# Kernel tuning notes

Hardware: AMD Instinct MI355X
Metric: run time of the kernel (lower is better)

Reference implementation:

```python
import jax, jax.numpy as jnp
import numpy as np

H, D, KV, S, PAST, BS, NB = 32, 128, 8, 128, 8064, 128, 128
T = PAST + S          # total context = 8192
NBLK = T // BS        # logical blocks used = 64
NEG = jnp.float32(-1e30)


def setup_inputs() -> dict:
    key = jax.random.key(0)
    ks = jax.random.split(key, 6)
    q = jax.random.normal(ks[0], (1, H, S, D), jnp.float32)
    k = jax.random.normal(ks[1], (1, KV, S, D), jnp.float32)
    v = jax.random.normal(ks[2], (1, KV, S, D), jnp.float32)
    pk = jax.random.normal(ks[3], (NB, KV, BS, D), jnp.float32)
    pv = jax.random.normal(ks[4], (NB, KV, BS, D), jnp.float32)
    # block table: 64 logical blocks mapped to distinct physical blocks (paged indirection)
    bt = jax.random.permutation(ks[5], NB)[:NBLK].astype(jnp.int32)
    return dict(
        query_state=q, key_state=k, value_state=v,
        attn_mask=jnp.ones((1,), jnp.float32),  # unused: causal prefill path (use_attention_mask=False)
        past_key_state=pk, past_value_state=pv,
        seq_position=PAST,
        scale=jnp.float32(1.0 / np.sqrt(D)),
        block_tables=bt, block_size=BS,
    )


def reference(query_state, key_state, value_state, attn_mask,
              past_key_state, past_value_state, seq_position, scale,
              block_tables, block_size):
    # phase == 'prefill', use_attention_mask=False -> paged_causal_attn_prefill
    kvh = past_key_state.shape[1]
    s_new = query_state.shape[2]
    total = seq_position + s_new  # static python int

    # --- append new K/V into the paged cache at positions [seq_position, total) ---
    pos_new = seq_position + jnp.arange(s_new)
    blk = block_tables[pos_new // block_size]
    off = pos_new % block_size
    k_new = jnp.transpose(key_state[0], (1, 0, 2))    # [S, KV, D]
    v_new = jnp.transpose(value_state[0], (1, 0, 2))
    kc = past_key_state.at[blk, :, off, :].set(k_new)
    vc = past_value_state.at[blk, :, off, :].set(v_new)

    # --- gather the full context [0, total) through the block table ---
    pos = jnp.arange(total)
    blk_a = block_tables[pos // block_size]
    off_a = pos % block_size
    K = kc[blk_a, :, off_a, :]   # [T, KV, D]
    V = vc[blk_a, :, off_a, :]

    # --- grouped-query causal attention ---
    g = query_state.shape[1] // kvh
    q = query_state.reshape(kvh, g, s_new, -1)                 # [KV, G, S, D]
    scores = jnp.einsum('kgsd,tkd->kgst', q, K) * scale        # [KV, G, S, T]
    causal = pos[None, :] <= (seq_position + jnp.arange(s_new))[:, None]  # [S, T]
    scores = jnp.where(causal[None, None], scores, NEG)
    probs = jax.nn.softmax(scores, axis=-1)
    out = jnp.einsum('kgst,tkd->kgsd', probs, V)               # [KV, G, S, D]

    h = kvh * g
    out = out.reshape(1, h, s_new, -1)                         # [1, H, S, D]
    out = jnp.transpose(out, (0, 2, 1, 3)).reshape(1, s_new, h * out.shape[-1])
    return out
```

## Files before the change

kernel.cpp:

```cpp
#include <hip/hip_runtime.h>
#include <hip/hip_bf16.h>


typedef unsigned short u16;
typedef unsigned int u32;
typedef __bf16 bf16x8 __attribute__((ext_vector_type(8)));
typedef float f32x16 __attribute__((ext_vector_type(16)));
typedef float f32x4 __attribute__((ext_vector_type(4)));
typedef u32 u32x4 __attribute__((ext_vector_type(4)));
typedef u32 u32x2 __attribute__((ext_vector_type(2)));
typedef int i32x2 __attribute__((ext_vector_type(2)));

#define NHEAD 32
#define DH 128
#define NKV 8
#define SQ 128
#define PAST_T 8064
#define TOTAL_T 8192
#define BK 64
#define KSTR 136
#define VT_SZ 8192
#define WSPP (16384 + 256)
#define MSUB 17.3123405f

__device__ __forceinline__ u32 pk2f(float lo, float hi) {
  union {
    __hip_bfloat162 b;
    u32 u;
  } cv;
  cv.b = __float22bfloat162_rn(make_float2(lo, hi));
  return cv.u;
}

template <int NPART>
__global__ __launch_bounds__(512, 1) void flash_part(
    const float* __restrict__ q, const float* __restrict__ knew,
    const float* __restrict__ vnew, const float* __restrict__ pk,
    const float* __restrict__ pv, const int* __restrict__ btab,
    const float* __restrict__ scp, float* __restrict__ ws) {
  constexpr int CHUNK = TOTAL_T / NPART;
  constexpr int NITER = CHUNK / BK;
  __shared__ __attribute__((aligned(16))) u16 k_s[2 * BK * KSTR];
  __shared__ __attribute__((aligned(16))) u16 vt_s[2 * VT_SZ];
  __shared__ int bt_s[64];

  const int bid = blockIdx.x;
  const int kv = bid & 7;
  const int t = bid >> 3;
  const int p = t % NPART;
  const int gp = t / NPART;

  const int tid = threadIdx.x;
  const int wid = tid >> 6;
  const int lane = tid & 63;
  const int g2 = wid & 1;
  const int w = wid >> 1;
  const int h = kv * 4 + gp * 2 + g2;
  const int l31 = lane & 31, grp = lane >> 5;
  const int pstart = p * CHUNK;

  if (tid < 64) bt_s[tid] = btab[tid];
  const float qs = scp[0] * 1.44269504f;

  u32x4 qf[8];
  {
    const float* qp = q + ((size_t)(h * SQ + w * 32 + l31)) * DH;
#pragma unroll
    for (int st = 0; st < 8; ++st) {
      const f32x4 a = *(const f32x4*)(qp + st * 16 + grp * 8);
      const f32x4 b = *(const f32x4*)(qp + st * 16 + grp * 8 + 4);
      u32x4 f;
      f[0] = pk2f(a[0] * qs, a[1] * qs);
      f[1] = pk2f(a[2] * qs, a[3] * qs);
      f[2] = pk2f(b[0] * qs, b[1] * qs);
      f[3] = pk2f(b[2] * qs, b[3] * qs);
      qf[st] = f;
    }
  }

  f32x16 oacc[4];
#pragma unroll
  for (int i = 0; i < 4; ++i)
#pragma unroll
    for (int rr = 0; rr < 16; ++rr) oacc[i][rr] = 0.0f;
  float l_acc = 0.0f;

  __syncthreads();

  f32x4 kr0, kr1, kr2, kr3;
  float va[8], vb[8];
  const int kc4 = (tid & 31) * 4;
  const int ktrow = tid >> 5;
  const int vd = tid & 127;
  const int tb8a = tid >> 7;
  const int vofA =
      ((((vd >> 5) * 4 + (tb8a >> 1)) * 2 + (tb8a & 1)) * 32 + (vd & 31)) * 8;
  const int vofB =
      ((((vd >> 5) * 4 + ((tb8a + 4) >> 1)) * 2 + ((tb8a + 4) & 1)) * 32 +
       (vd & 31)) * 8;

  auto load_tile = [&](int it) {
    const int t0 = pstart + it * BK;
    const float *sk, *sv;
    if (t0 < PAST_T) {
      const size_t boff =
          (((size_t)bt_s[t0 >> 7] * NKV + kv) * 128 + (t0 & 127)) * (size_t)DH;
      sk = pk + boff;
      sv = pv + boff;
    } else {
      const size_t noff = ((size_t)kv * SQ + (t0 - PAST_T)) * (size_t)DH;
      sk = knew + noff;
      sv = vnew + noff;
    }
    kr0 = *(const f32x4*)(sk + (size_t)(ktrow + 0) * DH + kc4);
    kr1 = *(const f32x4*)(sk + (size_t)(ktrow + 16) * DH + kc4);
    kr2 = *(const f32x4*)(sk + (size_t)(ktrow + 32) * DH + kc4);
    kr3 = *(const f32x4*)(sk + (size_t)(ktrow + 48) * DH + kc4);
#pragma unroll
    for (int j = 0; j < 8; ++j)
      va[j] = sv[(size_t)(tb8a * 8 + j) * DH + vd];
#pragma unroll
    for (int j = 0; j < 8; ++j)
      vb[j] = sv[(size_t)((tb8a + 4) * 8 + j) * DH + vd];
  };
  auto store_tile = [&](int buf) {
    u16* ks = k_s + buf * (BK * KSTR);
    u16* vs = vt_s + buf * VT_SZ;
    {
      u32x2 pw;
      pw[0] = pk2f(kr0[0], kr0[1]);
      pw[1] = pk2f(kr0[2], kr0[3]);
      *(u32x2*)&ks[(ktrow + 0) * KSTR + kc4] = pw;
    }
    {
      u32x2 pw;
      pw[0] = pk2f(kr1[0], kr1[1]);
      pw[1] = pk2f(kr1[2], kr1[3]);
      *(u32x2*)&ks[(ktrow + 16) * KSTR + kc4] = pw;
    }
    {
      u32x2 pw;
      pw[0] = pk2f(kr2[0], kr2[1]);
      pw[1] = pk2f(kr2[2], kr2[3]);
      *(u32x2*)&ks[(ktrow + 32) * KSTR + kc4] = pw;
    }
    {
      u32x2 pw;
      pw[0] = pk2f(kr3[0], kr3[1]);
      pw[1] = pk2f(kr3[2], kr3[3]);
      *(u32x2*)&ks[(ktrow + 48) * KSTR + kc4] = pw;
    }
    {
      u32x4 wa;
#pragma unroll
      for (int jj = 0; jj < 4; ++jj) wa[jj] = pk2f(va[2 * jj], va[2 * jj + 1]);
      *(u32x4*)&vs[vofA] = wa;
    }
    {
      u32x4 wb;
#pragma unroll
      for (int jj = 0; jj < 4; ++jj) wb[jj] = pk2f(vb[2 * jj], vb[2 * jj + 1]);
      *(u32x4*)&vs[vofB] = wb;
    }
  };

  load_tile(0);
  store_tile(0);
  __syncthreads();

  for (int it = 0; it < NITER; ++it) {
    const int buf = it & 1;
    if (it + 1 < NITER) load_tile(it + 1);

    const u16* ks = k_s + buf * (BK * KSTR);
    const u16* vs = vt_s + buf * VT_SZ;
    const int t0 = pstart + it * BK;
    const int qcol = w * 32 + l31;

    f32x16 sacc0, sacc1;
#pragma unroll
    for (int rr = 0; rr < 16; ++rr) sacc0[rr] = 0.0f;
#pragma unroll
    for (int rr = 0; rr < 16; ++rr) sacc1[rr] = 0.0f;
    __builtin_amdgcn_s_setprio(1);
#pragma unroll
    for (int st = 0; st < 8; ++st) {
      const u32x4 kf0 = *(const u32x4*)&ks[l31 * KSTR + st * 16 + grp * 8];
      sacc0 = __builtin_amdgcn_mfma_f32_32x32x16_bf16(
          __builtin_bit_cast(bf16x8, kf0), __builtin_bit_cast(bf16x8, qf[st]),
          sacc0, 0, 0, 0);
      const u32x4 kf1 =
          *(const u32x4*)&ks[(l31 + 32) * KSTR + st * 16 + grp * 8];
      sacc1 = __builtin_amdgcn_mfma_f32_32x32x16_bf16(
          __builtin_bit_cast(bf16x8, kf1), __builtin_bit_cast(bf16x8, qf[st]),
          sacc1, 0, 0, 0);
    }
    __builtin_amdgcn_s_setprio(0);

#pragma unroll
    for (int ts = 0; ts < 2; ++ts) {
      const f32x16& sacc = ts ? sacc1 : sacc0;
      const int tb = t0 + ts * 32;

      float pr[16];
      if (tb > PAST_T - 32) {
#pragma unroll
        for (int rr = 0; rr < 16; ++rr) {
          const int trow = (rr & 3) + 8 * (rr >> 2) + 4 * grp;
          const float e = __builtin_amdgcn_exp2f(sacc[rr] - MSUB);
          pr[rr] = ((tb + trow - PAST_T) > qcol) ? 0.0f : e;
        }
      } else {
#pragma unroll
        for (int rr = 0; rr < 16; ++rr)
          pr[rr] = __builtin_amdgcn_exp2f(sacc[rr] - MSUB);
      }
      float rs = 0.0f;
#pragma unroll
      for (int rr = 0; rr < 16; ++rr) rs += pr[rr];
      l_acc += rs;

      u32 pkk[8];
#pragma unroll
      for (int j = 0; j < 8; ++j) pkk[j] = pk2f(pr[2 * j], pr[2 * j + 1]);

      u32x4 pf1, pf2;
#if __has_builtin(__builtin_amdgcn_permlane32_swap)
      {
        const i32x2 s02 = __builtin_amdgcn_permlane32_swap(
            (int)pkk[0], (int)pkk[2], false, false);
        const i32x2 s13 = __builtin_amdgcn_permlane32_swap(
            (int)pkk[1], (int)pkk[3], false, false);
        const i32x2 s46 = __builtin_amdgcn_permlane32_swap(
            (int)pkk[4], (int)pkk[6], false, false);
        const i32x2 s57 = __builtin_amdgcn_permlane32_swap(
            (int)pkk[5], (int)pkk[7], false, false);
        pf1[0] = (u32)s02[0];
        pf1[1] = (u32)s13[0];
        pf1[2] = (u32)s02[1];
        pf1[3] = (u32)s13[1];
        pf2[0] = (u32)s46[0];
        pf2[1] = (u32)s57[0];
        pf2[2] = (u32)s46[1];
        pf2[3] = (u32)s57[1];
      }
#else
      {
        u32 xch[8];
#pragma unroll
        for (int j = 0; j < 8; ++j)
          xch[j] = (u32)__shfl_xor((int)pkk[j], 32, 64);
        pf1[0] = grp ? xch[2] : pkk[0];
        pf1[1] = grp ? xch[3] : pkk[1];
        pf1[2] = grp ? pkk[2] : xch[0];
        pf1[3] = grp ? pkk[3] : xch[1];
        pf2[0] = grp ? xch[6] : pkk[4];
        pf2[1] = grp ? xch[7] : pkk[5];
        pf2[2] = grp ? pkk[6] : xch[4];
        pf2[3] = grp ? pkk[7] : xch[5];
      }
#endif

      __builtin_amdgcn_s_setprio(1);
#pragma unroll
      for (int dt = 0; dt < 4; ++dt) {
        const u32x4 av =
            *(const u32x4*)&vs[((((dt * 4 + ts * 2) * 2 + grp) * 32 + l31)) * 8];
        oacc[dt] = __builtin_amdgcn_mfma_f32_32x32x16_bf16(
            __builtin_bit_cast(bf16x8, av), __builtin_bit_cast(bf16x8, pf1),
            oacc[dt], 0, 0, 0);
        const u32x4 bv =
            *(const u32x4*)&vs[((((dt * 4 + ts * 2 + 1) * 2 + grp) * 32 + l31)) *
                               8];
        oacc[dt] = __builtin_amdgcn_mfma_f32_32x32x16_bf16(
            __builtin_bit_cast(bf16x8, bv), __builtin_bit_cast(bf16x8, pf2),
            oacc[dt], 0, 0, 0);
      }
      __builtin_amdgcn_s_setprio(0);

      if (ts == 0 && it + 1 < NITER) store_tile(buf ^ 1);
    }

    __syncthreads();
  }

  float* wsp = ws + (size_t)(h * NPART + p) * WSPP;
#pragma unroll
  for (int dt = 0; dt < 4; ++dt)
#pragma unroll
    for (int rr = 0; rr < 16; ++rr) {
      const int dd = dt * 32 + (rr & 3) + 8 * (rr >> 2) + 4 * grp;
      wsp[dd * 128 + w * 32 + l31] = oacc[dt][rr];
    }
  const float l_tot = l_acc + __shfl_xor(l_acc, 32, 64);
  if (grp == 0) wsp[16384 + w * 32 + l31] = l_tot;
}

template <int NPART>
__global__ __launch_bounds__(256, 2) void combine_out(
    const float* __restrict__ ws, float* __restrict__ out) {
  __shared__ float rden_s[128];

  const int dblk = blockIdx.x;
  const int h = blockIdx.y;
  const int tid = threadIdx.x;
  const float* base = ws + (size_t)h * NPART * WSPP;

  if (tid < 128) {
    float denom = 0.0f;
#pragma unroll
    for (int pp = 0; pp < NPART; ++pp)
      denom += base[(size_t)pp * WSPP + 16384 + tid];
    rden_s[tid] = 1.0f / denom;
  }
  __syncthreads();

  const int qq = tid & 127;
  const int dp = tid >> 7;
  const int d0 = dblk * 4 + dp * 2;

  float a0 = 0.0f, a1 = 0.0f;
#pragma unroll
  for (int pp = 0; pp < NPART; ++pp) {
    const float* b = base + (size_t)pp * WSPP;
    a0 += b[d0 * 128 + qq];
    a1 += b[(d0 + 1) * 128 + qq];
  }
  const float r = rden_s[qq];
  float2 o;
  o.x = a0 * r;
  o.y = a1 * r;
  *(float2*)(out + (size_t)qq * (NHEAD * DH) + h * DH + d0) = o;
}

extern "C" void kernel_launch(void* const* d_in, const int* in_sizes, int n_in,
                              void* d_out, int out_size, void* d_ws,
                              size_t ws_size, hipStream_t stream) {
  const float* q = (const float*)d_in[0];
  const float* knew = (const float*)d_in[1];
  const float* vnew = (const float*)d_in[2];
  const float* pk = (const float*)d_in[4];
  const float* pv = (const float*)d_in[5];
  const float* scp = (const float*)d_in[7];
  const int* btab = (const int*)d_in[8];
  float* ws = (float*)d_ws;
  float* out = (float*)d_out;

  const size_t need16 = (size_t)NHEAD * 16 * WSPP * sizeof(float);
  const size_t need8 = (size_t)NHEAD * 8 * WSPP * sizeof(float);
  if (ws_size >= need16) {
    flash_part<16><<<dim3(8 * 2 * 16), 512, 0, stream>>>(q, knew, vnew, pk, pv,
                                                         btab, scp, ws);
    combine_out<16><<<dim3(32, NHEAD), 256, 0, stream>>>(ws, out);
  } else if (ws_size >= need8) {
    flash_part<8><<<dim3(8 * 2 * 8), 512, 0, stream>>>(q, knew, vnew, pk, pv,
                                                       btab, scp, ws);
    combine_out<8><<<dim3(32, NHEAD), 256, 0, stream>>>(ws, out);
  }
}
```

Baseline: 172.1 us.

## Remap flash-decode blocks: 4 heads per block, 32-key tiles, 24 uneven KV splits

Restructures the partitioned attention kernel so each 256-thread block handles one 32-query slice for all four GQA heads of a KV group, sharing each K/V tile across four waves instead of two. The key tile shrinks from 64 to 32 rows. The context is split into 24 uneven partitions of tiles, giving 768 blocks at up to 3 blocks per CU. The goal is to cut redundant K/V loads per head group and improve occupancy and load balance across CUs. The cost is more workspace, a larger combine, and a smaller tile per barrier.

Measured after the change: 209.4 us. +21.7%, slower.

```diff
diff --git a/kernel.cpp b/kernel.cpp
--- a/kernel.cpp
+++ b/kernel.cpp
@@ -17,9 +17,9 @@
 #define SQ 128
 #define PAST_T 8064
 #define TOTAL_T 8192
-#define BK 64
+#define BK 32
 #define KSTR 136
-#define VT_SZ 8192
+#define VT_SZ 4096
 #define WSPP (16384 + 256)
 #define MSUB 17.3123405f
 
@@ -33,38 +33,39 @@
 }
 
 template <int NPART>
-__global__ __launch_bounds__(512, 1) void flash_part(
+__global__ __launch_bounds__(256, 3) void flash_part(
     const float* __restrict__ q, const float* __restrict__ knew,
     const float* __restrict__ vnew, const float* __restrict__ pk,
     const float* __restrict__ pv, const int* __restrict__ btab,
     const float* __restrict__ scp, float* __restrict__ ws) {
-  constexpr int CHUNK = TOTAL_T / NPART;
-  constexpr int NITER = CHUNK / BK;
+  constexpr int TILES = TOTAL_T / BK;
+  constexpr int TBASE = TILES / NPART;
+  constexpr int TREM = TILES % NPART;
   __shared__ __attribute__((aligned(16))) u16 k_s[2 * BK * KSTR];
   __shared__ __attribute__((aligned(16))) u16 vt_s[2 * VT_SZ];
   __shared__ int bt_s[64];
 
   const int bid = blockIdx.x;
   const int kv = bid & 7;
-  const int t = bid >> 3;
-  const int p = t % NPART;
-  const int gp = t / NPART;
+  const int rest = bid >> 3;
+  const int qb = rest & 3;
+  const int p = rest >> 2;
+  const int ntile = TBASE + (p < TREM ? 1 : 0);
+  const int tile0 = p * TBASE + (p < TREM ? p : TREM);
 
   const int tid = threadIdx.x;
   const int wid = tid >> 6;
   const int lane = tid & 63;
-  const int g2 = wid & 1;
-  const int w = wid >> 1;
-  const int h = kv * 4 + gp * 2 + g2;
+  const int h = kv * 4 + wid;
   const int l31 = lane & 31, grp = lane >> 5;
-  const int pstart = p * CHUNK;
+  const int qcol = qb * 32 + l31;
 
   if (tid < 64) bt_s[tid] = btab[tid];
   const float qs = scp[0] * 1.44269504f;
 
   u32x4 qf[8];
   {
-    const float* qp = q + ((size_t)(h * SQ + w * 32 + l31)) * DH;
+    const float* qp = q + ((size_t)(h * SQ + qb * 32 + l31)) * DH;
 #pragma unroll
     for (int st = 0; st < 8; ++st) {
       const f32x4 a = *(const f32x4*)(qp + st * 16 + grp * 8);
@@ -88,19 +89,18 @@
   __syncthreads();
 
   f32x4 kr0, kr1, kr2, kr3;
-  float va[8], vb[8];
+  float va[16];
   const int kc4 = (tid & 31) * 4;
   const int ktrow = tid >> 5;
   const int vd = tid & 127;
-  const int tb8a = tid >> 7;
+  const int vhalf = tid >> 7;
   const int vofA =
-      ((((vd >> 5) * 4 + (tb8a >> 1)) * 2 + (tb8a & 1)) * 32 + (vd & 31)) * 8;
+      ((((vd >> 5) * 2 + vhalf) * 2 + 0) * 32 + (vd & 31)) * 8;
   const int vofB =
-      ((((vd >> 5) * 4 + ((tb8a + 4) >> 1)) * 2 + ((tb8a + 4) & 1)) * 32 +
-       (vd & 31)) * 8;
+      ((((vd >> 5) * 2 + vhalf) * 2 + 1) * 32 + (vd & 31)) * 8;
 
   auto load_tile = [&](int it) {
-    const int t0 = pstart + it * BK;
+    const int t0 = (tile0 + it) * BK;
     const float *sk, *sv;
     if (t0 < PAST_T) {
       const size_t boff =
@@ -113,15 +113,12 @@
       sv = vnew + noff;
     }
     kr0 = *(const f32x4*)(sk + (size_t)(ktrow + 0) * DH + kc4);
-    kr1 = *(const f32x4*)(sk + (size_t)(ktrow + 16) * DH + kc4);
-    kr2 = *(const f32x4*)(sk + (size_t)(ktrow + 32) * DH + kc4);
-    kr3 = *(const f32x4*)(sk + (size_t)(ktrow + 48) * DH + kc4);
-#pragma unroll
-    for (int j = 0; j < 8; ++j)
-      va[j] = sv[(size_t)(tb8a * 8 + j) * DH + vd];
-#pragma unroll
-    for (int j = 0; j < 8; ++j)
-      vb[j] = sv[(size_t)((tb8a + 4) * 8 + j) * DH + vd];
+    kr1 = *(const f32x4*)(sk + (size_t)(ktrow + 8) * DH + kc4);
+    kr2 = *(const f32x4*)(sk + (size_t)(ktrow + 16) * DH + kc4);
+    kr3 = *(const f32x4*)(sk + (size_t)(ktrow + 24) * DH + kc4);
+#pragma unroll
+    for (int j = 0; j < 16; ++j)
+      va[j] = sv[(size_t)(vhalf * 16 + j) * DH + vd];
   };
   auto store_tile = [&](int buf) {
     u16* ks = k_s + buf * (BK * KSTR);
@@ -136,19 +133,19 @@
       u32x2 pw;
       pw[0] = pk2f(kr1[0], kr1[1]);
       pw[1] = pk2f(kr1[2], kr1[3]);
-      *(u32x2*)&ks[(ktrow + 16) * KSTR + kc4] = pw;
+      *(u32x2*)&ks[(ktrow + 8) * KSTR + kc4] = pw;
     }
     {
       u32x2 pw;
       pw[0] = pk2f(kr2[0], kr2[1]);
       pw[1] = pk2f(kr2[2], kr2[3]);
-      *(u32x2*)&ks[(ktrow + 32) * KSTR + kc4] = pw;
+      *(u32x2*)&ks[(ktrow + 16) * KSTR + kc4] = pw;
     }
     {
       u32x2 pw;
       pw[0] = pk2f(kr3[0], kr3[1]);
       pw[1] = pk2f(kr3[2], kr3[3]);
-      *(u32x2*)&ks[(ktrow + 48) * KSTR + kc4] = pw;
+      *(u32x2*)&ks[(ktrow + 24) * KSTR + kc4] = pw;
     }
     {
       u32x4 wa;
@@ -159,7 +156,8 @@
     {
       u32x4 wb;
 #pragma unroll
-      for (int jj = 0; jj < 4; ++jj) wb[jj] = pk2f(vb[2 * jj], vb[2 * jj + 1]);
+      for (int jj = 0; jj < 4; ++jj)
+        wb[jj] = pk2f(va[8 + 2 * jj], va[9 + 2 * jj]);
       *(u32x4*)&vs[vofB] = wb;
     }
   };
@@ -168,119 +166,104 @@
   store_tile(0);
   __syncthreads();
 
-  for (int it = 0; it < NITER; ++it) {
+  for (int it = 0; it < ntile; ++it) {
     const int buf = it & 1;
-    if (it + 1 < NITER) load_tile(it + 1);
+    if (it + 1 < ntile) load_tile(it + 1);
 
     const u16* ks = k_s + buf * (BK * KSTR);
     const u16* vs = vt_s + buf * VT_SZ;
-    const int t0 = pstart + it * BK;
-    const int qcol = w * 32 + l31;
-
-    f32x16 sacc0, sacc1;
-#pragma unroll
-    for (int rr = 0; rr < 16; ++rr) sacc0[rr] = 0.0f;
-#pragma unroll
-    for (int rr = 0; rr < 16; ++rr) sacc1[rr] = 0.0f;
+    const int t0 = (tile0 + it) * BK;
+
+    f32x16 sacc;
+#pragma unroll
+    for (int rr = 0; rr < 16; ++rr) sacc[rr] = 0.0f;
     __builtin_amdgcn_s_setprio(1);
 #pragma unroll
     for (int st = 0; st < 8; ++st) {
-      const u32x4 kf0 = *(const u32x4*)&ks[l31 * KSTR + st * 16 + grp * 8];
-      sacc0 = __builtin_amdgcn_mfma_f32_32x32x16_bf16(
-          __builtin_bit_cast(bf16x8, kf0), __builtin_bit_cast(bf16x8, qf[st]),
-          sacc0, 0, 0, 0);
-      const u32x4 kf1 =
-          *(const u32x4*)&ks[(l31 + 32) * KSTR + st * 16 + grp * 8];
-      sacc1 = __builtin_amdgcn_mfma_f32_32x32x16_bf16(
-          __builtin_bit_cast(bf16x8, kf1), __builtin_bit_cast(bf16x8, qf[st]),
-          sacc1, 0, 0, 0);
+      const u32x4 kf = *(const u32x4*)&ks[l31 * KSTR + st * 16 + grp * 8];
+      sacc = __builtin_amdgcn_mfma_f32_32x32x16_bf16(
+          __builtin_bit_cast(bf16x8, kf), __builtin_bit_cast(bf16x8, qf[st]),
+          sacc, 0, 0, 0);
     }
     __builtin_amdgcn_s_setprio(0);
 
-#pragma unroll
-    for (int ts = 0; ts < 2; ++ts) {
-      const f32x16& sacc = ts ? sacc1 : sacc0;
-      const int tb = t0 + ts * 32;
-
-      float pr[16];
-      if (tb > PAST_T - 32) {
-#pragma unroll
-        for (int rr = 0; rr < 16; ++rr) {
-          const int trow = (rr & 3) + 8 * (rr >> 2) + 4 * grp;
-          const float e = __builtin_amdgcn_exp2f(sacc[rr] - MSUB);
-          pr[rr] = ((tb + trow - PAST_T) > qcol) ? 0.0f : e;
-        }
-      } else {
-#pragma unroll
-        for (int rr = 0; rr < 16; ++rr)
-          pr[rr] = __builtin_amdgcn_exp2f(sacc[rr] - MSUB);
+    float pr[16];
+    if (t0 > PAST_T - BK) {
+#pragma unroll
+      for (int rr = 0; rr < 16; ++rr) {
+        const int trow = (rr & 3) + 8 * (rr >> 2) + 4 * grp;
+        const float e = __builtin_amdgcn_exp2f(sacc[rr] - MSUB);
+        pr[rr] = ((t0 + trow - PAST_T) > qcol) ? 0.0f : e;
       }
-      float rs = 0.0f;
-#pragma unroll
-      for (int rr = 0; rr < 16; ++rr) rs += pr[rr];
-      l_acc += rs;
-
-      u32 pkk[8];
-#pragma unroll
-      for (int j = 0; j < 8; ++j) pkk[j] = pk2f(pr[2 * j], pr[2 * j + 1]);
-
-      u32x4 pf1, pf2;
+    } else {
+#pragma unroll
+      for (int rr = 0; rr < 16; ++rr)
+        pr[rr] = __builtin_amdgcn_exp2f(sacc[rr] - MSUB);
+    }
+    float rs = 0.0f;
+#pragma unroll
+    for (int rr = 0; rr < 16; ++rr) rs += pr[rr];
+    l_acc += rs;
+
+    u32 pkk[8];
+#pragma unroll
+    for (int j = 0; j < 8; ++j) pkk[j] = pk2f(pr[2 * j], pr[2 * j + 1]);
+
+    u32x4 pf1, pf2;
 #if __has_builtin(__builtin_amdgcn_permlane32_swap)
-      {
-        const i32x2 s02 = __builtin_amdgcn_permlane32_swap(
-            (int)pkk[0], (int)pkk[2], false, false);
-        const i32x2 s13 = __builtin_amdgcn_permlane32_swap(
-            (int)pkk[1], (int)pkk[3], false, false);
-        const i32x2 s46 = __builtin_amdgcn_permlane32_swap(
-            (int)pkk[4], (int)pkk[6], false, false);
-        const i32x2 s57 = __builtin_amdgcn_permlane32_swap(
-            (int)pkk[5], (int)pkk[7], false, false);
-        pf1[0] = (u32)s02[0];
-        pf1[1] = (u32)s13[0];
-        pf1[2] = (u32)s02[1];
-        pf1[3] = (u32)s13[1];
-        pf2[0] = (u32)s46[0];
-        pf2[1] = (u32)s57[0];
-        pf2[2] = (u32)s46[1];
-        pf2[3] = (u32)s57[1];
-      }
+    {
+      const i32x2 s02 = __builtin_amdgcn_permlane32_swap(
+          (int)pkk[0], (int)pkk[2], false, false);
+      const i32x2 s13 = __builtin_amdgcn_permlane32_swap(
+          (int)pkk[1], (int)pkk[3], false, false);
+      const i32x2 s46 = __builtin_amdgcn_permlane32_swap(
+          (int)pkk[4], (int)pkk[6], false, false);
+      const i32x2 s57 = __builtin_amdgcn_permlane32_swap(
+          (int)pkk[5], (int)pkk[7], false, false);
+      pf1[0] = (u32)s02[0];
+      pf1[1] = (u32)s13[0];
+      pf1[2] = (u32)s02[1];
+      pf1[3] = (u32)s13[1];
+      pf2[0] = (u32)s46[0];
+      pf2[1] = (u32)s57[0];
+      pf2[2] = (u32)s46[1];
+      pf2[3] = (u32)s57[1];
+    }
 #else
-      {
-        u32 xch[8];
-#pragma unroll
-        for (int j = 0; j < 8; ++j)
-          xch[j] = (u32)__shfl_xor((int)pkk[j], 32, 64);
-        pf1[0] = grp ? xch[2] : pkk[0];
-        pf1[1] = grp ? xch[3] : pkk[1];
-        pf1[2] = grp ? pkk[2] : xch[0];
-        pf1[3] = grp ? pkk[3] : xch[1];
-        pf2[0] = grp ? xch[6] : pkk[4];
-        pf2[1] = grp ? xch[7] : pkk[5];
-        pf2[2] = grp ? pkk[6] : xch[4];
-        pf2[3] = grp ? pkk[7] : xch[5];
-      }
+    {
+      u32 xch[8];
+#pragma unroll
+      for (int j = 0; j < 8; ++j) xch[j] = (u32)__shfl_xor((int)pkk[j], 32, 64);
+      pf1[0] = grp ? xch[2] : pkk[0];
+      pf1[1] = grp ? xch[3] : pkk[1];
+      pf1[2] = grp ? pkk[2] : xch[0];
+      pf1[3] = grp ? pkk[3] : xch[1];
+      pf2[0] = grp ? xch[6] : pkk[4];
+      pf2[1] = grp ? xch[7] : pkk[5];
+      pf2[2] = grp ? pkk[6] : xch[4];
+      pf2[3] = grp ? pkk[7] : xch[5];
+    }
 #endif
 
-      __builtin_amdgcn_s_setprio(1);
-#pragma unroll
-      for (int dt = 0; dt < 4; ++dt) {
-        const u32x4 av =
-            *(const u32x4*)&vs[((((dt * 4 + ts * 2) * 2 + grp) * 32 + l31)) * 8];
-        oacc[dt] = __builtin_amdgcn_mfma_f32_32x32x16_bf16(
-            __builtin_bit_cast(bf16x8, av), __builtin_bit_cast(bf16x8, pf1),
-            oacc[dt], 0, 0, 0);
-        const u32x4 bv =
-            *(const u32x4*)&vs[((((dt * 4 + ts * 2 + 1) * 2 + grp) * 32 + l31)) *
-                               8];
-        oacc[dt] = __builtin_amdgcn_mfma_f32_32x32x16_bf16(
-            __builtin_bit_cast(bf16x8, bv), __builtin_bit_cast(bf16x8, pf2),
-            oacc[dt], 0, 0, 0);
-      }
-      __builtin_amdgcn_s_setprio(0);
-
-      if (ts == 0 && it + 1 < NITER) store_tile(buf ^ 1);
-    }
-
+    __builtin_amdgcn_s_setprio(1);
+#pragma unroll
+    for (int dt = 0; dt < 4; ++dt) {
+      const u32x4 av =
+          *(const u32x4*)&vt_s[buf * VT_SZ +
+                               (((dt * 2 + 0) * 2 + grp) * 32 + l31) * 8];
+      oacc[dt] = __builtin_amdgcn_mfma_f32_32x32x16_bf16(
+          __builtin_bit_cast(bf16x8, av), __builtin_bit_cast(bf16x8, pf1),
+          oacc[dt], 0, 0, 0);
+      const u32x4 bv =
+          *(const u32x4*)&vt_s[buf * VT_SZ +
+                               (((dt * 2 + 1) * 2 + grp) * 32 + l31) * 8];
+      oacc[dt] = __builtin_amdgcn_mfma_f32_32x32x16_bf16(
+          __builtin_bit_cast(bf16x8, bv), __builtin_bit_cast(bf16x8, pf2),
+          oacc[dt], 0, 0, 0);
+    }
+    __builtin_amdgcn_s_setprio(0);
+
+    if (it + 1 < ntile) store_tile(buf ^ 1);
     __syncthreads();
   }
 
@@ -290,10 +273,10 @@
 #pragma unroll
     for (int rr = 0; rr < 16; ++rr) {
       const int dd = dt * 32 + (rr & 3) + 8 * (rr >> 2) + 4 * grp;
-      wsp[dd * 128 + w * 32 + l31] = oacc[dt][rr];
+      wsp[dd * 128 + qb * 32 + l31] = oacc[dt][rr];
     }
   const float l_tot = l_acc + __shfl_xor(l_acc, 32, 64);
-  if (grp == 0) wsp[16384 + w * 32 + l31] = l_tot;
+  if (grp == 0) wsp[16384 + qb * 32 + l31] = l_tot;
 }
 
 template <int NPART>
@@ -346,15 +329,15 @@
   float* ws = (float*)d_ws;
   float* out = (float*)d_out;
 
+  const size_t need24 = (size_t)NHEAD * 24 * WSPP * sizeof(float);
   const size_t need16 = (size_t)NHEAD * 16 * WSPP * sizeof(float);
-  const size_t need8 = (size_t)NHEAD * 8 * WSPP * sizeof(float);
-  if (ws_size >= need16) {
-    flash_part<16><<<dim3(8 * 2 * 16), 512, 0, stream>>>(q, knew, vnew, pk, pv,
+  if (ws_size >= need24) {
+    flash_part<24><<<dim3(8 * 4 * 24), 256, 0, stream>>>(q, knew, vnew, pk, pv,
+                                                         btab, scp, ws);
+    combine_out<24><<<dim3(32, NHEAD), 256, 0, stream>>>(ws, out);
+  } else if (ws_size >= need16) {
+    flash_part<16><<<dim3(8 * 4 * 16), 256, 0, stream>>>(q, knew, vnew, pk, pv,
                                                          btab, scp, ws);
     combine_out<16><<<dim3(32, NHEAD), 256, 0, stream>>>(ws, out);
-  } else if (ws_size >= need8) {
-    flash_part<8><<<dim3(8 * 2 * 8), 512, 0, stream>>>(q, knew, vnew, pk, pv,
-                                                       btab, scp, ws);
-    combine_out<8><<<dim3(32, NHEAD), 256, 0, stream>>>(ws, out);
   }
 }
```
